# Performance work log

Measured on AMD Instinct MI355X. Metric: run time of the kernel, lower is better.

Reference implementation:

```python
import jax, jax.numpy as jnp
import numpy as np

E = 2          # e_layers
DM = 64        # d_model == emb_dim (hardcoded 64 in out_layer)
H = 8          # n_heads
DH = DM // H
DFF = 256      # d_ff
P = 16         # patch_size
STRIDE = P // 2
SL = 4096      # seq_len
NPATCH = (SL - P) // STRIDE + 1   # 511
PRED = 96
B, M = 8, 8
FACTOR = 5
EPS = 1e-5


def setup_inputs() -> dict:
    key = jax.random.key(0)
    ks = jax.random.split(key, 32)
    s = jnp.float32(0.02)
    f = lambda i, shape: jax.random.normal(ks[i], shape, jnp.float32)
    d = {
        "x_enc": f(0, (B, SL, M)),
        "x_mark_enc": f(1, (B, SL, 4)),
        "x_dec": f(2, (B, PRED, M)),
        "x_mark_dec": f(3, (B, PRED, 4)),
        # patch embedding  Linear(patch_size -> emb_dim)
        "in_W": f(4, (DM, P)) * s,
        "in_b": jnp.zeros((DM,), jnp.float32),
        # per-layer attention projections (stacked over e_layers)
        "Wq": f(5, (E, DM, DM)) * s, "bq": jnp.zeros((E, DM), jnp.float32),
        "Wk": f(6, (E, DM, DM)) * s, "bk": jnp.zeros((E, DM), jnp.float32),
        "Wv": f(7, (E, DM, DM)) * s, "bv": jnp.zeros((E, DM), jnp.float32),
        "Wo": f(8, (E, DM, DM)) * s, "bo": jnp.zeros((E, DM), jnp.float32),
        # FFN (Conv1d kernel=1 == Linear)
        "c1_W": f(9, (E, DFF, DM)) * s, "c1_b": jnp.zeros((E, DFF), jnp.float32),
        "c2_W": f(10, (E, DM, DFF)) * s, "c2_b": jnp.zeros((E, DM), jnp.float32),
        # layer norms
        "ln1_g": jnp.ones((E, DM), jnp.float32), "ln1_b": jnp.zeros((E, DM), jnp.float32),
        "ln2_g": jnp.ones((E, DM), jnp.float32), "ln2_b": jnp.zeros((E, DM), jnp.float32),
        "lnf_g": jnp.ones((DM,), jnp.float32), "lnf_b": jnp.zeros((DM,), jnp.float32),
        # decode head  Linear(64*num_patches -> pred_len)
        "out_W": f(11, (PRED, DM * NPATCH)) * s,
        "out_b": jnp.zeros((PRED,), jnp.float32),
    }
    return d


def _ln(x, g, b):
    mu = x.mean(-1, keepdims=True)
    var = ((x - mu) ** 2).mean(-1, keepdims=True)
    return (x - mu) * jax.lax.rsqrt(var + EPS) * g + b


def _prob_attn(q, k, v, key):
    # q,k,v: [Bn, H, L, Dh]  (ProbSparse attention, mask_flag=False)
    Bn, h, Lq, Dh = q.shape
    Lk = k.shape[2]
    U_part = min(int(FACTOR * np.ceil(np.log(Lk))), Lk)   # sampled keys per query
    u = min(int(FACTOR * np.ceil(np.log(Lq))), Lq)        # top-u active queries
    idx = jax.random.randint(key, (Lq, U_part), 0, Lk)
    k_sample = k[:, :, idx, :]                             # [Bn,H,Lq,U,Dh]
    qk_sample = jnp.einsum('bhld,bhlud->bhlu', q, k_sample)
    # sparsity measure: max - sum/L_K (as in torch code)
    sparsity = qk_sample.max(-1) - qk_sample.sum(-1) / jnp.float32(Lk)
    _, top_idx = jax.lax.top_k(sparsity, u)                # [Bn,H,u]
    q_red = jnp.take_along_axis(q, top_idx[..., None], axis=2)  # [Bn,H,u,Dh]
    scale = jax.lax.rsqrt(jnp.float32(Dh))
    scores = jnp.einsum('bhud,bhkd->bhuk', q_red, k) * scale    # [Bn,H,u,Lk]
    attn = jax.nn.softmax(scores, axis=-1)
    # lazy context: mean of V for inactive queries, attn@V for active ones
    ctx = jnp.broadcast_to(v.mean(axis=2, keepdims=True), q.shape)
    upd = jnp.einsum('bhuk,bhkd->bhud', attn, v)
    bi = jnp.arange(Bn)[:, None, None]
    hi = jnp.arange(h)[None, :, None]
    ctx = ctx.at[bi, hi, top_idx].set(upd)
    return ctx.transpose(0, 2, 1, 3)  # [Bn,L,H,Dh]


def reference(x_enc, x_mark_enc, x_dec, x_mark_dec, in_W, in_b, Wq, bq, Wk, bk,
              Wv, bv, Wo, bo, c1_W, c1_b, c2_W, c2_b, ln1_g, ln1_b, ln2_g, ln2_b,
              lnf_g, lnf_b, out_W, out_b):
    Bb, L, Mm = x_enc.shape
    x = x_enc.transpose(0, 2, 1)  # b l m -> b m l
    pidx = jnp.arange(NPATCH)[:, None] * STRIDE + jnp.arange(P)[None, :]
    patches = x[:, :, pidx]                         # [B,M,N,P] (unfold)
    z = patches.reshape(Bb * Mm, NPATCH, P) @ in_W.T + in_b  # [BM,N,DM]
    akey = jax.random.key(1)
    for e in range(E):
        q = (z @ Wq[e].T + bq[e]).reshape(Bb * Mm, NPATCH, H, DH).transpose(0, 2, 1, 3)
        k = (z @ Wk[e].T + bk[e]).reshape(Bb * Mm, NPATCH, H, DH).transpose(0, 2, 1, 3)
        v = (z @ Wv[e].T + bv[e]).reshape(Bb * Mm, NPATCH, H, DH).transpose(0, 2, 1, 3)
        ctx = _prob_attn(q, k, v, jax.random.fold_in(akey, e))
        new_x = ctx.reshape(Bb * Mm, NPATCH, DM) @ Wo[e].T + bo[e]
        x1 = _ln(z + new_x, ln1_g[e], ln1_b[e])
        y = jax.nn.gelu(x1 @ c1_W[e].T + c1_b[e], approximate=False)
        y = y @ c2_W[e].T + c2_b[e]
        z = _ln(x1 + y, ln2_g[e], ln2_b[e])
    z = _ln(z, lnf_g, lnf_b)
    out = z.reshape(Bb * Mm, -1) @ out_W.T + out_b   # [BM, pred_len]
    out = out.reshape(Bb, Mm, PRED).transpose(0, 2, 1)  # (b m) l -> b l m
    return out[:, -PRED:, :]
```

## Files before the change

kernel.cpp:

```cpp
#include <hip/hip_runtime.h>
#include <hip/hip_bf16.h>
#include <stdint.h>
#include <math.h>

typedef __hip_bfloat16 bf16;
typedef __attribute__((ext_vector_type(8))) short short8;
typedef __attribute__((ext_vector_type(4))) short short4v;
typedef __attribute__((ext_vector_type(4))) float fx4;

#define NP 511
#define UPART 35
#define NTOK 32704
#define NBITS 17885
#define LN_EPS 1e-5f

__host__ __device__ __forceinline__ void tf2x32(uint32_t k0, uint32_t k1,
                                                uint32_t x0, uint32_t x1,
                                                uint32_t* o0, uint32_t* o1) {
  uint32_t ks2 = k0 ^ k1 ^ 0x1BD11BDAu;
  x0 += k0; x1 += k1;
#define TFR(r) { x0 += x1; x1 = (x1 << (r)) | (x1 >> (32 - (r))); x1 ^= x0; }
  TFR(13) TFR(15) TFR(26) TFR(6)   x0 += k1;  x1 += ks2 + 1u;
  TFR(17) TFR(29) TFR(16) TFR(24)  x0 += ks2; x1 += k0 + 2u;
  TFR(13) TFR(15) TFR(26) TFR(6)   x0 += k0;  x1 += k1 + 3u;
  TFR(17) TFR(29) TFR(16) TFR(24)  x0 += k1;  x1 += ks2 + 4u;
  TFR(13) TFR(15) TFR(26) TFR(6)   x0 += ks2; x1 += k0 + 5u;
#undef TFR
  *o0 = x0; *o1 = x1;
}

__device__ __forceinline__ float ldin(const void* p, int i, int f32) {
  if (f32) return ((const float*)p)[i];
  return __bfloat162float(((const bf16*)p)[i]);
}
__device__ __forceinline__ unsigned short f2bf(float v) {
  uint32_t u = __builtin_bit_cast(uint32_t, v);
  u += 0x7fffu + ((u >> 16) & 1u);
  return (unsigned short)(u >> 16);
}
__device__ __forceinline__ float bfb2f(uint32_t h) {
  uint32_t u = h << 16;
  return __builtin_bit_cast(float, u);
}
__device__ __forceinline__ float lo16(uint32_t w) { return bfb2f(w & 0xFFFFu); }
__device__ __forceinline__ float hi16(uint32_t w) { return bfb2f(w >> 16); }
__device__ __forceinline__ uint32_t pack2(float a, float b) {
  return (uint32_t)f2bf(a) | ((uint32_t)f2bf(b) << 16);
}
__device__ __forceinline__ int lanes_below(unsigned long long m) {
  return __builtin_amdgcn_mbcnt_hi((uint32_t)(m >> 32),
         __builtin_amdgcn_mbcnt_lo((uint32_t)m, 0));
}

__global__ void zero_out_kernel(bf16* __restrict__ out, int n) {
  int i = blockIdx.x * 256 + threadIdx.x;
  if (i < n) out[i] = __float2bfloat16(0.f);
}

__global__ void gen_idx_kernel(int* __restrict__ idxT,
    uint32_t ka0, uint32_t ka1, uint32_t kb0, uint32_t kb1,
    const uint32_t* __restrict__ lnfg, int* __restrict__ flag) {
  if (blockIdx.x == 0 && threadIdx.x == 0)
    flag[0] = (lnfg[0] == 0x3F800000u) ? 1 : 0;
  int i = blockIdx.x * 256 + threadIdx.x;
  if (i >= 2 * NBITS) return;
  int e = i / NBITS;
  uint32_t j = (uint32_t)(i - e * NBITS);
  uint32_t k0 = e ? kb0 : ka0, k1 = e ? kb1 : ka1;
  uint32_t o0, o1;
  tf2x32(k0, k1, 0u, j, &o0, &o1);
  uint32_t bits = o1;
  uint32_t hi = bits >> 16, lo = bits & 0xFFFFu;
  uint32_t off = ((hi % 511u) * 32u + (lo % 511u)) % 511u;
  int l = (int)(j / UPART), u = (int)(j % UPART);
  idxT[e * NBITS + u * NP + l] = (int)off;
}

__global__ __launch_bounds__(256) void embed_kernel(
    const void* __restrict__ xe, const void* __restrict__ inW,
    const void* __restrict__ inb, float* __restrict__ z,
    const int* __restrict__ flg) {
  __shared__ float xs[136 * 8];
  int f = flg[0];
  int b = blockIdx.x >> 5, nt = blockIdx.x & 31;
  int n0 = nt * 16;
  for (int i = threadIdx.x; i < 1088; i += 256) {
    int row = i >> 3, m = i & 7;
    int g = n0 * 8 + row;
    xs[i] = (g < 4096) ? ldin(xe, (b * 4096 + g) * 8 + m, f) : 0.f;
  }
  int d = threadIdx.x & 63, mg = threadIdx.x >> 6;
  float wreg[16];
#pragma unroll
  for (int p = 0; p < 16; ++p) wreg[p] = ldin(inW, d * 16 + p, f);
  float bd = ldin(inb, d, f);
  __syncthreads();
  for (int nl = 0; nl < 16; ++nl) {
    int n = n0 + nl;
    if (n >= NP) break;
#pragma unroll
    for (int mm = 0; mm < 2; ++mm) {
      int m = mg * 2 + mm;
      float acc = bd;
#pragma unroll
      for (int p = 0; p < 16; ++p)
        acc = fmaf(xs[(nl * 8 + p) * 8 + m], wreg[p], acc);
      int t = (b * 8 + m) * NP + n;
      z[(size_t)t * 64 + d] = acc;
    }
  }
}

__global__ __launch_bounds__(256) void qkv_kernel(
    const float* __restrict__ z,
    const void* __restrict__ Wq, const void* __restrict__ bq,
    const void* __restrict__ Wk, const void* __restrict__ bk,
    const void* __restrict__ Wv, const void* __restrict__ bv,
    bf16* __restrict__ qb, bf16* __restrict__ kb, bf16* __restrict__ vb,
    const int* __restrict__ flg, int e) {
  __shared__ short xb[64 * 72];
  __shared__ short wL[192 * 72];
  __shared__ float bqs[192];
  int f = flg[0];
  int t0 = blockIdx.x * 64;
  int tid = threadIdx.x;
  {
    const float4* xg = (const float4*)(z + (size_t)t0 * 64);
#pragma unroll
    for (int r = 0; r < 4; ++r) {
      int i4 = r * 256 + tid;
      float4 v = xg[i4];
      int t = (i4 * 4) >> 6, d = (i4 * 4) & 63;
      short4v h;
      h.x = (short)f2bf(v.x); h.y = (short)f2bf(v.y);
      h.z = (short)f2bf(v.z); h.w = (short)f2bf(v.w);
      *(short4v*)&xb[t * 72 + d] = h;
    }
  }
  if (!f) {
    const uint4* Wg0 = (const uint4*)((const bf16*)Wq + e * 4096);
    const uint4* Wg1 = (const uint4*)((const bf16*)Wk + e * 4096);
    const uint4* Wg2 = (const uint4*)((const bf16*)Wv + e * 4096);
#pragma unroll
    for (int r = 0; r < 2; ++r) {
      int i = r * 256 + tid;
      int row = i >> 3, c8 = (i & 7) * 8;
      *(uint4*)&wL[row * 72 + c8] = Wg0[i];
      *(uint4*)&wL[(64 + row) * 72 + c8] = Wg1[i];
      *(uint4*)&wL[(128 + row) * 72 + c8] = Wg2[i];
    }
  } else {
#pragma unroll
    for (int r = 0; r < 16; ++r) {
      int i = r * 256 + tid;
      int row = i >> 6, c = i & 63;
      wL[row * 72 + c] = (short)f2bf(((const float*)Wq)[e * 4096 + i]);
      wL[(64 + row) * 72 + c] = (short)f2bf(((const float*)Wk)[e * 4096 + i]);
      wL[(128 + row) * 72 + c] = (short)f2bf(((const float*)Wv)[e * 4096 + i]);
    }
  }
  if (tid < 192) {
    int t3 = tid >> 6, j = tid & 63;
    bqs[tid] = (t3 == 0) ? ldin(bq, e * 64 + j, f)
             : (t3 == 1) ? ldin(bk, e * 64 + j, f)
                         : ldin(bv, e * 64 + j, f);
  }
  __syncthreads();
  int lane = tid & 63, w = tid >> 6;
  int m0 = w * 16, col = lane & 15, quad = lane >> 4;
  short8 a0 = *(const short8*)&xb[(m0 + col) * 72 + quad * 8];
  short8 a1 = *(const short8*)&xb[(m0 + col) * 72 + 32 + quad * 8];
#pragma unroll
  for (int nt = 0; nt < 12; ++nt) {
    fx4 acc = {0.f, 0.f, 0.f, 0.f};
    short8 b0 = *(const short8*)&wL[(nt * 16 + col) * 72 + quad * 8];
    short8 b1 = *(const short8*)&wL[(nt * 16 + col) * 72 + 32 + quad * 8];
    acc = __builtin_amdgcn_mfma_f32_16x16x32_bf16(a0, b0, acc, 0, 0, 0);
    acc = __builtin_amdgcn_mfma_f32_16x16x32_bf16(a1, b1, acc, 0, 0, 0);
    int c = nt * 16 + col;
    int t3 = c >> 6, hd = c & 63, h = hd >> 3, d2 = hd & 7;
    bf16* base = (t3 == 0) ? qb : (t3 == 1) ? kb : vb;
    float bia = bqs[c];
#pragma unroll
    for (int reg = 0; reg < 4; ++reg) {
      int tok = t0 + m0 + quad * 4 + reg;
      int bm = tok / NP, n = tok - bm * NP;
      base[((size_t)(bm * 8 + h) * NP + n) * 8 + d2] =
          __float2bfloat16(acc[reg] + bia);
    }
  }
}

__global__ __launch_bounds__(1024, 8) void attn_fused_kernel(
    const bf16* __restrict__ qg, const bf16* __restrict__ kg,
    const bf16* __restrict__ vg, const int* __restrict__ idxT,
    bf16* __restrict__ ctx) {
  __shared__ uint32_t kkp[NP * 5 + 5];
  __shared__ uint32_t kvp[NP * 5 + 5];
  __shared__ float spars[512];
  __shared__ float mxB_s[512], smB_s[512];
  __shared__ float redv[256];
  __shared__ int topi[UPART];
  __shared__ float vmean[8];
  __shared__ unsigned char selflag[NP + 1];
  int bh = blockIdx.x;
  int bm = bh >> 3, h = bh & 7;
  size_t hb = (size_t)bh * NP * 8;
  int tid = threadIdx.x;
  int lane = tid & 63, wv = tid >> 6;
  if (tid < 512) {
    if (tid < NP) {
      uint4 b = ((const uint4*)(kg + hb))[tid];
      uint32_t* dk = kkp + tid * 5;
      dk[0] = b.x; dk[1] = b.y; dk[2] = b.z; dk[3] = b.w;
    }
  } else {
    int n = tid - 512;
    if (n < NP) {
      uint4 c = ((const uint4*)(vg + hb))[n];
      uint32_t* dv = kvp + n * 5;
      dv[0] = c.x; dv[1] = c.y; dv[2] = c.z; dv[3] = c.w;
    }
  }
  __syncthreads();
  float mxA = -1e30f, smA = 0.f;
  if (tid < NP) {
    int l = tid;
    uint4 a = ((const uint4*)(qg + hb))[l];
    float ql[8];
    ql[0] = lo16(a.x); ql[1] = hi16(a.x);
    ql[2] = lo16(a.y); ql[3] = hi16(a.y);
    ql[4] = lo16(a.z); ql[5] = hi16(a.z);
    ql[6] = lo16(a.w); ql[7] = hi16(a.w);
#pragma unroll 6
    for (int u = 0; u < 18; ++u) {
      int j = idxT[u * NP + l];
      j = ((unsigned)j > 510u) ? 0 : j;
      const uint32_t* kr = kkp + j * 5;
      uint32_t w0 = kr[0], w1 = kr[1], w2 = kr[2], w3 = kr[3];
      float dt = 0.f;
      dt = fmaf(ql[0], lo16(w0), dt); dt = fmaf(ql[1], hi16(w0), dt);
      dt = fmaf(ql[2], lo16(w1), dt); dt = fmaf(ql[3], hi16(w1), dt);
      dt = fmaf(ql[4], lo16(w2), dt); dt = fmaf(ql[5], hi16(w2), dt);
      dt = fmaf(ql[6], lo16(w3), dt); dt = fmaf(ql[7], hi16(w3), dt);
      mxA = fmaxf(mxA, dt); smA += dt;
    }
  } else if (tid >= 512 && tid < 512 + NP) {
    int l = tid - 512;
    uint4 a = ((const uint4*)(qg + hb))[l];
    float ql[8];
    ql[0] = lo16(a.x); ql[1] = hi16(a.x);
    ql[2] = lo16(a.y); ql[3] = hi16(a.y);
    ql[4] = lo16(a.z); ql[5] = hi16(a.z);
    ql[6] = lo16(a.w); ql[7] = hi16(a.w);
    float mxB = -1e30f, smB = 0.f;
#pragma unroll 6
    for (int u = 18; u < 35; ++u) {
      int j = idxT[u * NP + l];
      j = ((unsigned)j > 510u) ? 0 : j;
      const uint32_t* kr = kkp + j * 5;
      uint32_t w0 = kr[0], w1 = kr[1], w2 = kr[2], w3 = kr[3];
      float dt = 0.f;
      dt = fmaf(ql[0], lo16(w0), dt); dt = fmaf(ql[1], hi16(w0), dt);
      dt = fmaf(ql[2], lo16(w1), dt); dt = fmaf(ql[3], hi16(w1), dt);
      dt = fmaf(ql[4], lo16(w2), dt); dt = fmaf(ql[5], hi16(w2), dt);
      dt = fmaf(ql[6], lo16(w3), dt); dt = fmaf(ql[7], hi16(w3), dt);
      mxB = fmaxf(mxB, dt); smB += dt;
    }
    mxB_s[l] = mxB; smB_s[l] = smB;
  }
  __syncthreads();
  if (tid < NP) {
    spars[tid] = fmaxf(mxA, mxB_s[tid]) - (smA + smB_s[tid]) * (1.0f / 511.0f);
  } else if (tid >= 512 && tid < 768) {
    int tt = tid - 512;
    int d = tt & 7, pt = tt >> 3;
    int c = d >> 1, odd = d & 1;
    float s = 0.f;
    for (int n = pt; n < NP; n += 32) {
      uint32_t w = kvp[n * 5 + c];
      s += odd ? hi16(w) : lo16(w);
    }
    redv[tt] = s;
  }
  __syncthreads();
  if (tid < 64) {
    uint32_t key[8];
#pragma unroll
    for (int jj = 0; jj < 8; ++jj) {
      int ll = lane + jj * 64;
      if (ll < NP) {
        uint32_t u = __builtin_bit_cast(uint32_t, spars[ll]);
        key[jj] = (u & 0x80000000u) ? ~u : (u | 0x80000000u);
      } else key[jj] = 0u;
    }
    uint32_t p = 0u;
    for (int b = 31; b >= 0; --b) {
      uint32_t t = p | (1u << b);
      int cnt = 0;
#pragma unroll
      for (int jj = 0; jj < 8; ++jj)
        cnt += __popcll(__ballot(key[jj] >= t));
      if (cnt >= UPART) p = t;
    }
    int c1 = 0;
#pragma unroll
    for (int jj = 0; jj < 8; ++jj)
      c1 += __popcll(__ballot(key[jj] > p));
    int need = UPART - c1;
    int base = 0, taken = 0;
#pragma unroll
    for (int jj = 0; jj < 8; ++jj) {
      int ll = lane + jj * 64;
      bool gt = key[jj] > p;
      bool eq = key[jj] == p;
      unsigned long long meq = __ballot(eq);
      int beq = lanes_below(meq);
      bool sel = gt || (eq && (taken + beq) < need);
      unsigned long long msel = __ballot(sel);
      int pos = base + lanes_below(msel);
      if (sel) topi[pos] = ll;
      if (ll < NP) selflag[ll] = sel ? 1 : 0;
      base += __popcll(msel);
      taken += __popcll(meq);
    }
  } else if (tid >= 64 && tid < 72) {
    int d = tid - 64;
    float s = 0.f;
#pragma unroll
    for (int pt = 0; pt < 32; ++pt) s += redv[pt * 8 + d];
    vmean[d] = s * (1.0f / 511.0f);
  }
  __syncthreads();
  size_t cb = (size_t)bm * (NP * 64) + h * 8;
  if (tid < NP && !selflag[tid]) {
    uint4 pv;
    pv.x = pack2(vmean[0], vmean[1]);
    pv.y = pack2(vmean[2], vmean[3]);
    pv.z = pack2(vmean[4], vmean[5]);
    pv.w = pack2(vmean[6], vmean[7]);
    *(uint4*)(ctx + cb + (size_t)tid * 64) = pv;
  }
  const float scale = 0.35355339059327373f;
  int l0 = topi[wv];
  int l1 = topi[wv + 16];
  bool has3 = (wv + 32) < UPART;
  int l2 = has3 ? topi[wv + 32] : l0;
  l0 = ((unsigned)l0 > 510u) ? 0 : l0;
  l1 = ((unsigned)l1 > 510u) ? 0 : l1;
  l2 = ((unsigned)l2 > 510u) ? 0 : l2;
  const uint4* q4p = (const uint4*)(qg + hb);
  uint4 qv0 = q4p[l0];
  uint4 qv1 = q4p[l1];
  uint4 qv2 = q4p[l2];

  auto process = [&](uint4 a, int lsel) {
    float qs[8];
    qs[0] = lo16(a.x); qs[1] = hi16(a.x);
    qs[2] = lo16(a.y); qs[3] = hi16(a.y);
    qs[4] = lo16(a.z); qs[5] = hi16(a.z);
    qs[6] = lo16(a.w); qs[7] = hi16(a.w);
    float sreg[8];
    float mx = -1e30f;
#pragma unroll
    for (int s = 0; s < 8; ++s) {
      int j = lane + s * 64;
      int jc = (j > 510) ? 0 : j;
      const uint32_t* kr = kkp + jc * 5;
      uint32_t w0 = kr[0], w1 = kr[1], w2 = kr[2], w3 = kr[3];
      float d0 = qs[0] * lo16(w0);
      d0 = fmaf(qs[1], hi16(w0), d0);
      d0 = fmaf(qs[2], lo16(w1), d0);
      d0 = fmaf(qs[3], hi16(w1), d0);
      float d1 = qs[4] * lo16(w2);
      d1 = fmaf(qs[5], hi16(w2), d1);
      d1 = fmaf(qs[6], lo16(w3), d1);
      d1 = fmaf(qs[7], hi16(w3), d1);
      float sc = (d0 + d1) * scale;
      sreg[s] = (j > 510) ? -1e30f : sc;
      mx = fmaxf(mx, sreg[s]);
    }
    for (int off = 32; off; off >>= 1) mx = fmaxf(mx, __shfl_xor(mx, off));
    float ssum = 0.f, acc[8];
#pragma unroll
    for (int d2 = 0; d2 < 8; ++d2) acc[d2] = 0.f;
#pragma unroll
    for (int s = 0; s < 8; ++s) {
      int j = lane + s * 64;
      int jc = (j > 510) ? 0 : j;
      float w = __expf(sreg[s] - mx);
      ssum += w;
      const uint32_t* vr = kvp + jc * 5;
      uint32_t x0 = vr[0], x1 = vr[1], x2 = vr[2], x3 = vr[3];
      acc[0] = fmaf(w, lo16(x0), acc[0]); acc[1] = fmaf(w, hi16(x0), acc[1]);
      acc[2] = fmaf(w, lo16(x1), acc[2]); acc[3] = fmaf(w, hi16(x1), acc[3]);
      acc[4] = fmaf(w, lo16(x2), acc[4]); acc[5] = fmaf(w, hi16(x2), acc[5]);
      acc[6] = fmaf(w, lo16(x3), acc[6]); acc[7] = fmaf(w, hi16(x3), acc[7]);
    }
    for (int off = 32; off; off >>= 1) {
      ssum += __shfl_xor(ssum, off);
#pragma unroll
      for (int d2 = 0; d2 < 8; ++d2) acc[d2] += __shfl_xor(acc[d2], off);
    }
    if (lane == 0) {
      float inv = 1.0f / ssum;
      uint4 pv;
      pv.x = pack2(acc[0] * inv, acc[1] * inv);
      pv.y = pack2(acc[2] * inv, acc[3] * inv);
      pv.z = pack2(acc[4] * inv, acc[5] * inv);
      pv.w = pack2(acc[6] * inv, acc[7] * inv);
      *(uint4*)(ctx + cb + (size_t)lsel * 64) = pv;
    }
  };
  process(qv0, l0);
  process(qv1, l1);
  if (has3) process(qv2, l2);
}

__global__ __launch_bounds__(256) void oproj_ffn_kernel(
    const float* __restrict__ z, const bf16* __restrict__ ctx,
    const void* __restrict__ Wo, const void* __restrict__ bo,
    const void* __restrict__ l1g, const void* __restrict__ l1b,
    const void* __restrict__ W1, const void* __restrict__ b1,
    const void* __restrict__ W2, const void* __restrict__ b2,
    const void* __restrict__ g, const void* __restrict__ bb,
    float* __restrict__ zo, bf16* __restrict__ zfT,
    const void* __restrict__ lfg, const void* __restrict__ lfb,
    const int* __restrict__ flg, int e, int last) {
  __shared__ __align__(16) char smem[73728];
  short* cbL = (short*)smem;
  short* woL = (short*)(smem + 9216);
  float* zf  = (float*)(smem + 18432);
  short* wA  = (short*)smem;
  short* rB  = (short*)(smem + 36864);
  float* b1s = (float*)(smem + 70656);
  float* b2s  = b1s + 256;
  float* gs   = b2s + 64;
  float* bbs  = gs + 64;
  float* g2s  = bbs + 64;
  float* bb2s = g2s + 64;
  float* bos  = bb2s + 64;
  float* g1s  = bos + 64;
  float* bb1s = g1s + 64;
  int f = flg[0];
  int t0 = blockIdx.x * 64;
  int tid = threadIdx.x;
  {
    const uint4* cg = (const uint4*)(ctx + (size_t)t0 * 64);
#pragma unroll
    for (int r = 0; r < 2; ++r) {
      int i = r * 256 + tid;
      uint4 v = cg[i];
      int row = i >> 3, c8 = (i & 7) * 8;
      *(uint4*)&cbL[row * 72 + c8] = v;
    }
    const float4* zg = (const float4*)(z + (size_t)t0 * 64);
#pragma unroll
    for (int r = 0; r < 4; ++r) {
      int i4 = r * 256 + tid;
      float4 v = zg[i4];
      int t = (i4 * 4) >> 6, d = (i4 * 4) & 63;
      *(float4*)&zf[t * 64 + d] = v;
    }
  }
  if (!f) {
    const uint4* Wg = (const uint4*)((const bf16*)Wo + e * 4096);
#pragma unroll
    for (int r = 0; r < 2; ++r) {
      int i = r * 256 + tid;
      int row = i >> 3, c8 = (i & 7) * 8;
      *(uint4*)&woL[row * 72 + c8] = Wg[i];
    }
  } else {
#pragma unroll
    for (int r = 0; r < 16; ++r) {
      int i = r * 256 + tid;
      int row = i >> 6, c = i & 63;
      woL[row * 72 + c] = (short)f2bf(((const float*)Wo)[e * 4096 + i]);
    }
  }
  b1s[tid] = ldin(b1, e * 256 + tid, f);
  if (tid < 64) {
    b2s[tid] = ldin(b2, e * 64 + tid, f);
    gs[tid] = ldin(g, e * 64 + tid, f);
    bbs[tid] = ldin(bb, e * 64 + tid, f);
    g2s[tid] = ldin(lfg, tid, f);
    bb2s[tid] = ldin(lfb, tid, f);
    bos[tid] = ldin(bo, e * 64 + tid, f);
    g1s[tid] = ldin(l1g, e * 64 + tid, f);
    bb1s[tid] = ldin(l1b, e * 64 + tid, f);
  }
  __syncthreads();
  int lane = tid & 63, w = tid >> 6;
  int m0 = w * 16, col = lane & 15, quad = lane >> 4;
  float x1v[4][4];
  {
    short8 a0 = *(const short8*)&cbL[(m0 + col) * 72 + quad * 8];
    short8 a1 = *(const short8*)&cbL[(m0 + col) * 72 + 32 + quad * 8];
    fx4 vacc[4];
#pragma unroll
    for (int nt = 0; nt < 4; ++nt) {
      fx4 acc = {0.f, 0.f, 0.f, 0.f};
      short8 b0 = *(const short8*)&woL[(nt * 16 + col) * 72 + quad * 8];
      short8 b1f = *(const short8*)&woL[(nt * 16 + col) * 72 + 32 + quad * 8];
      acc = __builtin_amdgcn_mfma_f32_16x16x32_bf16(a0, b0, acc, 0, 0, 0);
      acc = __builtin_amdgcn_mfma_f32_16x16x32_bf16(a1, b1f, acc, 0, 0, 0);
      vacc[nt] = acc;
    }
    float vals[4][4];
    float ps[4], sq[4];
#pragma unroll
    for (int reg = 0; reg < 4; ++reg) { ps[reg] = 0.f; sq[reg] = 0.f; }
#pragma unroll
    for (int nt = 0; nt < 4; ++nt) {
      int d = nt * 16 + col;
#pragma unroll
      for (int reg = 0; reg < 4; ++reg) {
        int tl = m0 + quad * 4 + reg;
        float v = vacc[nt][reg] + bos[d] + zf[tl * 64 + d];
        vals[nt][reg] = v;
        ps[reg] += v; sq[reg] += v * v;
      }
    }
#pragma unroll
    for (int off = 1; off < 16; off <<= 1) {
#pragma unroll
      for (int reg = 0; reg < 4; ++reg) {
        ps[reg] += __shfl_xor(ps[reg], off);
        sq[reg] += __shfl_xor(sq[reg], off);
      }
    }
#pragma unroll
    for (int reg = 0; reg < 4; ++reg) {
      float mu = ps[reg] * (1.0f / 64.0f);
      float var = sq[reg] * (1.0f / 64.0f) - mu * mu;
      float rs = rsqrtf(fmaxf(var, 0.f) + LN_EPS);
#pragma unroll
      for (int nt = 0; nt < 4; ++nt) {
        int d = nt * 16 + col;
        x1v[nt][reg] = (vals[nt][reg] - mu) * rs * g1s[d] + bb1s[d];
      }
    }
#pragma unroll
    for (int nt = 0; nt < 4; ++nt) {
#pragma unroll
      for (int reg = 0; reg < 4; ++reg) {
        int tl = m0 + quad * 4 + reg;
        rB[tl * 72 + nt * 16 + col] = (short)f2bf(x1v[nt][reg]);
      }
    }
  }
  __syncthreads();
  if (!f) {
    const uint4* W1g = (const uint4*)((const bf16*)W1 + e * 16384);
#pragma unroll
    for (int r = 0; r < 8; ++r) {
      int i = r * 256 + tid;
      uint4 v = W1g[i];
      int j = i >> 3, k = (i & 7) * 8;
      *(uint4*)&wA[j * 72 + k] = v;
    }
  } else {
    for (int r = 0; r < 64; ++r) {
      int i = r * 256 + tid;
      int j = i >> 6, k = i & 63;
      wA[j * 72 + k] = (short)f2bf(((const float*)W1)[e * 16384 + i]);
    }
  }
  short8 a0 = *(const short8*)&rB[(m0 + col) * 72 + quad * 8];
  short8 a1 = *(const short8*)&rB[(m0 + col) * 72 + 32 + quad * 8];
  __syncthreads();
#pragma unroll 4
  for (int nt = 0; nt < 16; ++nt) {
    fx4 acc = {0.f, 0.f, 0.f, 0.f};
    short8 bf0 = *(const short8*)&wA[(nt * 16 + col) * 72 + quad * 8];
    short8 bf1 = *(const short8*)&wA[(nt * 16 + col) * 72 + 32 + quad * 8];
    acc = __builtin_amdgcn_mfma_f32_16x16x32_bf16(a0, bf0, acc, 0, 0, 0);
    acc = __builtin_amdgcn_mfma_f32_16x16x32_bf16(a1, bf1, acc, 0, 0, 0);
    int j = nt * 16 + col;
    float bj = b1s[j];
#pragma unroll
    for (int reg = 0; reg < 4; ++reg) {
      float a = acc[reg] + bj;
      float ge = 0.5f * a * (1.0f + erff(a * 0.70710678118654752f));
      rB[(m0 + quad * 4 + reg) * 264 + j] = (short)f2bf(ge);
    }
  }
  __syncthreads();
  if (!f) {
    const uint4* W2g = (const uint4*)((const bf16*)W2 + e * 16384);
#pragma unroll
    for (int r = 0; r < 8; ++r) {
      int i = r * 256 + tid;
      uint4 v2 = W2g[i];
      int dd = i >> 5, c = (i & 31) * 8;
      *(uint4*)&wA[dd * 264 + c] = v2;
    }
  } else {
    for (int r = 0; r < 64; ++r) {
      int i = r * 256 + tid;
      int dd = i >> 8, c = i & 255;
      wA[dd * 264 + c] = (short)f2bf(((const float*)W2)[e * 16384 + i]);
    }
  }
  __syncthreads();
  short8 af[8];
#pragma unroll
  for (int kt = 0; kt < 8; ++kt)
    af[kt] = *(const short8*)&rB[(m0 + col) * 264 + kt * 32 + quad * 8];
  fx4 vacc[4];
#pragma unroll
  for (int nt = 0; nt < 4; ++nt) {
    fx4 acc = {0.f, 0.f, 0.f, 0.f};
#pragma unroll
    for (int kt = 0; kt < 8; ++kt) {
      short8 bfr = *(const short8*)&wA[(nt * 16 + col) * 264 + kt * 32 + quad * 8];
      acc = __builtin_amdgcn_mfma_f32_16x16x32_bf16(af[kt], bfr, acc, 0, 0, 0);
    }
    vacc[nt] = acc;
  }
  float vals[4][4];
  float ps[4], sq[4];
#pragma unroll
  for (int reg = 0; reg < 4; ++reg) { ps[reg] = 0.f; sq[reg] = 0.f; }
#pragma unroll
  for (int nt = 0; nt < 4; ++nt) {
    int d = nt * 16 + col;
#pragma unroll
    for (int reg = 0; reg < 4; ++reg) {
      float v = vacc[nt][reg] + b2s[d] + x1v[nt][reg];
      vals[nt][reg] = v;
      ps[reg] += v; sq[reg] += v * v;
    }
  }
#pragma unroll
  for (int off = 1; off < 16; off <<= 1) {
#pragma unroll
    for (int reg = 0; reg < 4; ++reg) {
      ps[reg] += __shfl_xor(ps[reg], off);
      sq[reg] += __shfl_xor(sq[reg], off);
    }
  }
  if (!last) {
#pragma unroll
    for (int reg = 0; reg < 4; ++reg) {
      float mu = ps[reg] * (1.0f / 64.0f);
      float var = sq[reg] * (1.0f / 64.0f) - mu * mu;
      float rs = rsqrtf(fmaxf(var, 0.f) + LN_EPS);
      int tl = m0 + quad * 4 + reg;
#pragma unroll
      for (int nt = 0; nt < 4; ++nt) {
        int d = nt * 16 + col;
        zo[(size_t)(t0 + tl) * 64 + d] = (vals[nt][reg] - mu) * rs * gs[d] + bbs[d];
      }
    }
  } else {
    float ps2[4], sq2[4];
#pragma unroll
    for (int reg = 0; reg < 4; ++reg) { ps2[reg] = 0.f; sq2[reg] = 0.f; }
    float v2s[4][4];
#pragma unroll
    for (int reg = 0; reg < 4; ++reg) {
      float mu = ps[reg] * (1.0f / 64.0f);
      float var = sq[reg] * (1.0f / 64.0f) - mu * mu;
      float rs = rsqrtf(fmaxf(var, 0.f) + LN_EPS);
#pragma unroll
      for (int nt = 0; nt < 4; ++nt) {
        int d = nt * 16 + col;
        float v2 = (vals[nt][reg] - mu) * rs * gs[d] + bbs[d];
        v2s[nt][reg] = v2;
        ps2[reg] += v2; sq2[reg] += v2 * v2;
      }
    }
#pragma unroll
    for (int off = 1; off < 16; off <<= 1) {
#pragma unroll
      for (int reg = 0; reg < 4; ++reg) {
        ps2[reg] += __shfl_xor(ps2[reg], off);
        sq2[reg] += __shfl_xor(sq2[reg], off);
      }
    }
#pragma unroll
    for (int reg = 0; reg < 4; ++reg) {
      float mu = ps2[reg] * (1.0f / 64.0f);
      float var = sq2[reg] * (1.0f / 64.0f) - mu * mu;
      float rs = rsqrtf(fmaxf(var, 0.f) + LN_EPS);
      int tok = t0 + m0 + quad * 4 + reg;
      int bm = tok / NP, n = tok - bm * NP;
#pragma unroll
      for (int nt = 0; nt < 4; ++nt) {
        int d = nt * 16 + col;
        zfT[(size_t)n * 4096 + bm * 64 + d] =
            __float2bfloat16((v2s[nt][reg] - mu) * rs * g2s[d] + bb2s[d]);
      }
    }
  }
}

__global__ __launch_bounds__(256) void head1_kernel(
    const bf16* __restrict__ zfT, const void* __restrict__ W,
    float* __restrict__ partial, const int* __restrict__ flg) {
  __shared__ short aL[64 * 72];
  __shared__ short bL[96 * 72];
  int f = flg[0];
  int n = blockIdx.x;
  int tid = threadIdx.x;
  {
    const uint4* Ag = (const uint4*)(zfT + (size_t)n * 4096);
#pragma unroll
    for (int r = 0; r < 2; ++r) {
      int i = r * 256 + tid;
      uint4 v = Ag[i];
      int row = i >> 3, c = (i & 7) * 8;
      *(uint4*)&aL[row * 72 + c] = v;
    }
  }
  if (!f) {
    const uint4* Wg = (const uint4*)W;
#pragma unroll
    for (int r = 0; r < 3; ++r) {
      int i = r * 256 + tid;
      int p = i >> 3, c8 = i & 7;
      uint4 v = Wg[(size_t)p * 4088 + n * 8 + c8];
      *(uint4*)&bL[p * 72 + c8 * 8] = v;
    }
  } else {
    for (int r = 0; r < 24; ++r) {
      int i = r * 256 + tid;
      int p = i >> 6, c = i & 63;
      bL[p * 72 + c] = (short)f2bf(((const float*)W)[(size_t)p * 32704 + n * 64 + c]);
    }
  }
  __syncthreads();
  int lane = tid & 63, w = tid >> 6;
  int m0 = w * 16, col = lane & 15, quad = lane >> 4;
  short8 a0 = *(const short8*)&aL[(m0 + col) * 72 + quad * 8];
  short8 a1 = *(const short8*)&aL[(m0 + col) * 72 + 32 + quad * 8];
  float* pb = partial + (size_t)n * 6144;
#pragma unroll
  for (int nt = 0; nt < 6; ++nt) {
    fx4 acc = {0.f, 0.f, 0.f, 0.f};
    short8 b0 = *(const short8*)&bL[(nt * 16 + col) * 72 + quad * 8];
    short8 b1 = *(const short8*)&bL[(nt * 16 + col) * 72 + 32 + quad * 8];
    acc = __builtin_amdgcn_mfma_f32_16x16x32_bf16(a0, b0, acc, 0, 0, 0);
    acc = __builtin_amdgcn_mfma_f32_16x16x32_bf16(a1, b1, acc, 0, 0, 0);
#pragma unroll
    for (int reg = 0; reg < 4; ++reg)
      pb[(m0 + quad * 4 + reg) * 96 + nt * 16 + col] = acc[reg];
  }
}

__global__ __launch_bounds__(256) void head2_kernel(
    const float* __restrict__ partial, const void* __restrict__ bias,
    void* __restrict__ out, const int* __restrict__ flg) {
  __shared__ float red[4][64];
  int f = flg[0];
  int lane = threadIdx.x & 63, w = threadIdx.x >> 6;
  int j = blockIdx.x * 64 + lane;
  float acc = 0.f;
  for (int n = w; n < NP; n += 4)
    acc += partial[(size_t)n * 6144 + j];
  red[w][lane] = acc;
  __syncthreads();
  if (w == 0) {
    float s = red[0][lane] + red[1][lane] + red[2][lane] + red[3][lane];
    int bm = j / 96, p = j - bm * 96;
    float val = s + ldin(bias, p, f);
    int b = bm >> 3, m = bm & 7;
    int o = (b * 96 + p) * 8 + m;
    if (f) ((float*)out)[o] = val;
    else   ((bf16*)out)[o] = __float2bfloat16(val);
  }
}

extern "C" void kernel_launch(void* const* d_in, const int* in_sizes, int n_in,
                              void* d_out, int out_size, void* d_ws, size_t ws_size,
                              hipStream_t stream) {
  const void* xe  = d_in[0];
  const void* inW = d_in[4];
  const void* inb = d_in[5];
  const void* Wq  = d_in[6];
  const void* bq  = d_in[7];
  const void* Wk  = d_in[8];
  const void* bk  = d_in[9];
  const void* Wv  = d_in[10];
  const void* bv  = d_in[11];
  const void* Wo  = d_in[12];
  const void* bo  = d_in[13];
  const void* c1W = d_in[14];
  const void* c1b = d_in[15];
  const void* c2W = d_in[16];
  const void* c2b = d_in[17];
  const void* l1g = d_in[18];
  const void* l1b = d_in[19];
  const void* l2g = d_in[20];
  const void* l2b = d_in[21];
  const void* lfg = d_in[22];
  const void* lfb = d_in[23];
  const void* oW  = d_in[24];
  const void* obv = d_in[25];

  const size_t NF = (size_t)NTOK * 64;
  const size_t REQ = (3 * NF + 2 * NBITS + 32) * sizeof(float);
  if (ws_size < REQ) {
    zero_out_kernel<<<(out_size + 255) / 256, 256, 0, stream>>>((bf16*)d_out, out_size);
    return;
  }

  float* z   = (float*)d_ws;
  bf16* ctxb = (bf16*)(z + NF);
  bf16* qb   = (bf16*)(z + NF + NF / 2);
  bf16* kb   = (bf16*)(z + 2 * NF);
  bf16* vb   = (bf16*)(z + 2 * NF + NF / 2);
  int* idxb  = (int*)(z + 3 * NF);
  int* flg   = idxb + 2 * NBITS;
  bf16* zfT  = ctxb;
  float* partial = z;

  uint32_t ke[2][2];
  for (int e = 0; e < 2; ++e)
    tf2x32(0u, 1u, 0u, (uint32_t)e, &ke[e][0], &ke[e][1]);
  gen_idx_kernel<<<(2 * NBITS + 255) / 256, 256, 0, stream>>>(idxb,
      ke[0][0], ke[0][1], ke[1][0], ke[1][1], (const uint32_t*)lfg, flg);

  embed_kernel<<<256, 256, 0, stream>>>(xe, inW, inb, z, flg);
  for (int e = 0; e < 2; ++e) {
    qkv_kernel<<<NTOK / 64, 256, 0, stream>>>(z, Wq, bq, Wk, bk, Wv, bv,
        qb, kb, vb, flg, e);
    attn_fused_kernel<<<512, 1024, 0, stream>>>(qb, kb, vb, idxb + e * NBITS,
        ctxb);
    oproj_ffn_kernel<<<NTOK / 64, 256, 0, stream>>>(z, ctxb, Wo, bo, l1g, l1b,
        c1W, c1b, c2W, c2b, l2g, l2b, z, zfT, lfg, lfb, flg, e, e == 1);
  }
  head1_kernel<<<NP, 256, 0, stream>>>(zfT, oW, partial, flg);
  head2_kernel<<<96, 256, 0, stream>>>(partial, obv, d_out, flg);
}
```

Measured before the change: 298.6 us.

## Merge index generation into embed kernel and halve FFN shared memory footprint

Fuses the random index generation kernel with the patch embedding kernel into one launch, with each block recomputing the dtype flag itself instead of reading it from a prior kernel. The O-proj+FFN kernel keeps the residual z in registers instead of staging it in shared memory. It also splits the W1 and W2 weight loads into two halves of 128 hidden units so LDS drops from 72KB to about 38KB, and adds launch bounds targeting 4 blocks per CU. This trades extra barriers and weight reloads for higher occupancy and one fewer launch.

```diff
diff --git a/kernel.cpp b/kernel.cpp
--- a/kernel.cpp
+++ b/kernel.cpp
@@ -12,6 +12,7 @@
 #define UPART 35
 #define NTOK 32704
 #define NBITS 17885
+#define GENB 140
 #define LN_EPS 1e-5f
 
 __host__ __device__ __forceinline__ void tf2x32(uint32_t k0, uint32_t k1,
@@ -57,32 +58,33 @@
   if (i < n) out[i] = __float2bfloat16(0.f);
 }
 
-__global__ void gen_idx_kernel(int* __restrict__ idxT,
+__global__ __launch_bounds__(256) void genidx_embed_kernel(
+    int* __restrict__ idxT,
     uint32_t ka0, uint32_t ka1, uint32_t kb0, uint32_t kb1,
-    const uint32_t* __restrict__ lnfg, int* __restrict__ flag) {
-  if (blockIdx.x == 0 && threadIdx.x == 0)
-    flag[0] = (lnfg[0] == 0x3F800000u) ? 1 : 0;
-  int i = blockIdx.x * 256 + threadIdx.x;
-  if (i >= 2 * NBITS) return;
-  int e = i / NBITS;
-  uint32_t j = (uint32_t)(i - e * NBITS);
-  uint32_t k0 = e ? kb0 : ka0, k1 = e ? kb1 : ka1;
-  uint32_t o0, o1;
-  tf2x32(k0, k1, 0u, j, &o0, &o1);
-  uint32_t bits = o1;
-  uint32_t hi = bits >> 16, lo = bits & 0xFFFFu;
-  uint32_t off = ((hi % 511u) * 32u + (lo % 511u)) % 511u;
-  int l = (int)(j / UPART), u = (int)(j % UPART);
-  idxT[e * NBITS + u * NP + l] = (int)off;
-}
-
-__global__ __launch_bounds__(256) void embed_kernel(
+    const uint32_t* __restrict__ lnfg, int* __restrict__ flag,
     const void* __restrict__ xe, const void* __restrict__ inW,
-    const void* __restrict__ inb, float* __restrict__ z,
-    const int* __restrict__ flg) {
+    const void* __restrict__ inb, float* __restrict__ z) {
+  if (blockIdx.x < GENB) {
+    if (blockIdx.x == 0 && threadIdx.x == 0)
+      flag[0] = (lnfg[0] == 0x3F800000u) ? 1 : 0;
+    int i = blockIdx.x * 256 + threadIdx.x;
+    if (i >= 2 * NBITS) return;
+    int e = i / NBITS;
+    uint32_t j = (uint32_t)(i - e * NBITS);
+    uint32_t k0 = e ? kb0 : ka0, k1 = e ? kb1 : ka1;
+    uint32_t o0, o1;
+    tf2x32(k0, k1, 0u, j, &o0, &o1);
+    uint32_t bits = o1;
+    uint32_t hi = bits >> 16, lo = bits & 0xFFFFu;
+    uint32_t off = ((hi % 511u) * 32u + (lo % 511u)) % 511u;
+    int l = (int)(j / UPART), u = (int)(j % UPART);
+    idxT[e * NBITS + u * NP + l] = (int)off;
+    return;
+  }
   __shared__ float xs[136 * 8];
-  int f = flg[0];
-  int b = blockIdx.x >> 5, nt = blockIdx.x & 31;
+  int f = (lnfg[0] == 0x3F800000u) ? 1 : 0;
+  int bid = blockIdx.x - GENB;
+  int b = bid >> 5, nt = bid & 31;
   int n0 = nt * 16;
   for (int i = threadIdx.x; i < 1088; i += 256) {
     int row = i >> 3, m = i & 7;
@@ -417,7 +419,7 @@
   if (has3) process(qv2, l2);
 }
 
-__global__ __launch_bounds__(256) void oproj_ffn_kernel(
+__global__ __launch_bounds__(256, 4) void oproj_ffn_kernel(
     const float* __restrict__ z, const bf16* __restrict__ ctx,
     const void* __restrict__ Wo, const void* __restrict__ bo,
     const void* __restrict__ l1g, const void* __restrict__ l1b,
@@ -427,13 +429,12 @@
     float* __restrict__ zo, bf16* __restrict__ zfT,
     const void* __restrict__ lfg, const void* __restrict__ lfb,
     const int* __restrict__ flg, int e, int last) {
-  __shared__ __align__(16) char smem[73728];
+  __shared__ __align__(16) char smem[38400];
   short* cbL = (short*)smem;
   short* woL = (short*)(smem + 9216);
-  float* zf  = (float*)(smem + 18432);
   short* wA  = (short*)smem;
-  short* rB  = (short*)(smem + 36864);
-  float* b1s = (float*)(smem + 70656);
+  short* rB  = (short*)(smem + 18432);
+  float* b1s = (float*)(smem + 35328);
   float* b2s  = b1s + 256;
   float* gs   = b2s + 64;
   float* bbs  = gs + 64;
@@ -445,6 +446,17 @@
   int f = flg[0];
   int t0 = blockIdx.x * 64;
   int tid = threadIdx.x;
+  int lane = tid & 63, w = tid >> 6;
+  int m0 = w * 16, col = lane & 15, quad = lane >> 4;
+  float zres[4][4];
+  {
+    const float* zp = z + ((size_t)(t0 + m0 + quad * 4)) * 64 + col;
+#pragma unroll
+    for (int nt = 0; nt < 4; ++nt)
+#pragma unroll
+      for (int reg = 0; reg < 4; ++reg)
+        zres[nt][reg] = zp[(size_t)reg * 64 + nt * 16];
+  }
   {
     const uint4* cg = (const uint4*)(ctx + (size_t)t0 * 64);
 #pragma unroll
@@ -453,14 +465,6 @@
       uint4 v = cg[i];
       int row = i >> 3, c8 = (i & 7) * 8;
       *(uint4*)&cbL[row * 72 + c8] = v;
-    }
-    const float4* zg = (const float4*)(z + (size_t)t0 * 64);
-#pragma unroll
-    for (int r = 0; r < 4; ++r) {
-      int i4 = r * 256 + tid;
-      float4 v = zg[i4];
-      int t = (i4 * 4) >> 6, d = (i4 * 4) & 63;
-      *(float4*)&zf[t * 64 + d] = v;
     }
   }
   if (!f) {
@@ -491,8 +495,6 @@
     bb1s[tid] = ldin(l1b, e * 64 + tid, f);
   }
   __syncthreads();
-  int lane = tid & 63, w = tid >> 6;
-  int m0 = w * 16, col = lane & 15, quad = lane >> 4;
   float x1v[4][4];
   {
     short8 a0 = *(const short8*)&cbL[(m0 + col) * 72 + quad * 8];
@@ -516,8 +518,7 @@
       int d = nt * 16 + col;
 #pragma unroll
       for (int reg = 0; reg < 4; ++reg) {
-        int tl = m0 + quad * 4 + reg;
-        float v = vacc[nt][reg] + bos[d] + zf[tl * 64 + d];
+        float v = vacc[nt][reg] + bos[d] + zres[nt][reg];
         vals[nt][reg] = v;
         ps[reg] += v; sq[reg] += v * v;
       }
@@ -551,71 +552,138 @@
     }
   }
   __syncthreads();
+  short8 ax0 = *(const short8*)&rB[(m0 + col) * 72 + quad * 8];
+  short8 ax1 = *(const short8*)&rB[(m0 + col) * 72 + 32 + quad * 8];
   if (!f) {
     const uint4* W1g = (const uint4*)((const bf16*)W1 + e * 16384);
 #pragma unroll
-    for (int r = 0; r < 8; ++r) {
+    for (int r = 0; r < 4; ++r) {
       int i = r * 256 + tid;
       uint4 v = W1g[i];
       int j = i >> 3, k = (i & 7) * 8;
       *(uint4*)&wA[j * 72 + k] = v;
     }
   } else {
-    for (int r = 0; r < 64; ++r) {
+    for (int r = 0; r < 32; ++r) {
       int i = r * 256 + tid;
       int j = i >> 6, k = i & 63;
       wA[j * 72 + k] = (short)f2bf(((const float*)W1)[e * 16384 + i]);
     }
   }
-  short8 a0 = *(const short8*)&rB[(m0 + col) * 72 + quad * 8];
-  short8 a1 = *(const short8*)&rB[(m0 + col) * 72 + 32 + quad * 8];
-  __syncthreads();
+  __syncthreads();
+  short* ysH = rB;
 #pragma unroll 4
-  for (int nt = 0; nt < 16; ++nt) {
+  for (int nt = 0; nt < 8; ++nt) {
     fx4 acc = {0.f, 0.f, 0.f, 0.f};
     short8 bf0 = *(const short8*)&wA[(nt * 16 + col) * 72 + quad * 8];
     short8 bf1 = *(const short8*)&wA[(nt * 16 + col) * 72 + 32 + quad * 8];
-    acc = __builtin_amdgcn_mfma_f32_16x16x32_bf16(a0, bf0, acc, 0, 0, 0);
-    acc = __builtin_amdgcn_mfma_f32_16x16x32_bf16(a1, bf1, acc, 0, 0, 0);
+    acc = __builtin_amdgcn_mfma_f32_16x16x32_bf16(ax0, bf0, acc, 0, 0, 0);
+    acc = __builtin_amdgcn_mfma_f32_16x16x32_bf16(ax1, bf1, acc, 0, 0, 0);
     int j = nt * 16 + col;
     float bj = b1s[j];
 #pragma unroll
     for (int reg = 0; reg < 4; ++reg) {
       float a = acc[reg] + bj;
       float ge = 0.5f * a * (1.0f + erff(a * 0.70710678118654752f));
-      rB[(m0 + quad * 4 + reg) * 264 + j] = (short)f2bf(ge);
-    }
-  }
-  __syncthreads();
+      ysH[(m0 + quad * 4 + reg) * 132 + j] = (short)f2bf(ge);
+    }
+  }
+  __syncthreads();
+  short8 af[8];
+#pragma unroll
+  for (int kt = 0; kt < 4; ++kt)
+    af[kt] = *(const short8*)&ysH[(m0 + col) * 132 + kt * 32 + quad * 8];
+  if (!f) {
+    const uint4* W1g = (const uint4*)((const bf16*)W1 + e * 16384 + 8192);
+#pragma unroll
+    for (int r = 0; r < 4; ++r) {
+      int i = r * 256 + tid;
+      uint4 v = W1g[i];
+      int j = i >> 3, k = (i & 7) * 8;
+      *(uint4*)&wA[j * 72 + k] = v;
+    }
+  } else {
+    for (int r = 0; r < 32; ++r) {
+      int i = r * 256 + tid;
+      int j = i >> 6, k = i & 63;
+      wA[j * 72 + k] = (short)f2bf(((const float*)W1)[e * 16384 + 8192 + i]);
+    }
+  }
+  __syncthreads();
+#pragma unroll 4
+  for (int nt = 0; nt < 8; ++nt) {
+    fx4 acc = {0.f, 0.f, 0.f, 0.f};
+    short8 bf0 = *(const short8*)&wA[(nt * 16 + col) * 72 + quad * 8];
+    short8 bf1 = *(const short8*)&wA[(nt * 16 + col) * 72 + 32 + quad * 8];
+    acc = __builtin_amdgcn_mfma_f32_16x16x32_bf16(ax0, bf0, acc, 0, 0, 0);
+    acc = __builtin_amdgcn_mfma_f32_16x16x32_bf16(ax1, bf1, acc, 0, 0, 0);
+    int jl = nt * 16 + col;
+    float bj = b1s[128 + jl];
+#pragma unroll
+    for (int reg = 0; reg < 4; ++reg) {
+      float a = acc[reg] + bj;
+      float ge = 0.5f * a * (1.0f + erff(a * 0.70710678118654752f));
+      ysH[(m0 + quad * 4 + reg) * 132 + jl] = (short)f2bf(ge);
+    }
+  }
+  __syncthreads();
+#pragma unroll
+  for (int kt = 0; kt < 4; ++kt)
+    af[4 + kt] = *(const short8*)&ysH[(m0 + col) * 132 + kt * 32 + quad * 8];
   if (!f) {
     const uint4* W2g = (const uint4*)((const bf16*)W2 + e * 16384);
 #pragma unroll
-    for (int r = 0; r < 8; ++r) {
-      int i = r * 256 + tid;
-      uint4 v2 = W2g[i];
-      int dd = i >> 5, c = (i & 31) * 8;
-      *(uint4*)&wA[dd * 264 + c] = v2;
+    for (int r = 0; r < 4; ++r) {
+      int i = r * 256 + tid;
+      int dd = i >> 4, c16 = i & 15;
+      uint4 v = W2g[dd * 32 + c16];
+      *(uint4*)&wA[dd * 132 + c16 * 8] = v;
     }
   } else {
-    for (int r = 0; r < 64; ++r) {
-      int i = r * 256 + tid;
-      int dd = i >> 8, c = i & 255;
-      wA[dd * 264 + c] = (short)f2bf(((const float*)W2)[e * 16384 + i]);
-    }
-  }
-  __syncthreads();
-  short8 af[8];
-#pragma unroll
-  for (int kt = 0; kt < 8; ++kt)
-    af[kt] = *(const short8*)&rB[(m0 + col) * 264 + kt * 32 + quad * 8];
+    for (int r = 0; r < 32; ++r) {
+      int i = r * 256 + tid;
+      int dd = i >> 7, cl = i & 127;
+      wA[dd * 132 + cl] = (short)f2bf(((const float*)W2)[e * 16384 + dd * 256 + cl]);
+    }
+  }
+  __syncthreads();
   fx4 vacc[4];
 #pragma unroll
   for (int nt = 0; nt < 4; ++nt) {
     fx4 acc = {0.f, 0.f, 0.f, 0.f};
 #pragma unroll
-    for (int kt = 0; kt < 8; ++kt) {
-      short8 bfr = *(const short8*)&wA[(nt * 16 + col) * 264 + kt * 32 + quad * 8];
+    for (int kt = 0; kt < 4; ++kt) {
+      short8 bfr = *(const short8*)&wA[(nt * 16 + col) * 132 + kt * 32 + quad * 8];
       acc = __builtin_amdgcn_mfma_f32_16x16x32_bf16(af[kt], bfr, acc, 0, 0, 0);
+    }
+    vacc[nt] = acc;
+  }
+  __syncthreads();
+  if (!f) {
+    const uint4* W2g = (const uint4*)((const bf16*)W2 + e * 16384);
+#pragma unroll
+    for (int r = 0; r < 4; ++r) {
+      int i = r * 256 + tid;
+      int dd = i >> 4, c16 = i & 15;
+      uint4 v = W2g[dd * 32 + 16 + c16];
+      *(uint4*)&wA[dd * 132 + c16 * 8] = v;
+    }
+  } else {
+    for (int r = 0; r < 32; ++r) {
+      int i = r * 256 + tid;
+      int dd = i >> 7, cl = i & 127;
+      wA[dd * 132 + cl] =
+          (short)f2bf(((const float*)W2)[e * 16384 + dd * 256 + 128 + cl]);
+    }
+  }
+  __syncthreads();
+#pragma unroll
+  for (int nt = 0; nt < 4; ++nt) {
+    fx4 acc = vacc[nt];
+#pragma unroll
+    for (int kt = 0; kt < 4; ++kt) {
+      short8 bfr = *(const short8*)&wA[(nt * 16 + col) * 132 + kt * 32 + quad * 8];
+      acc = __builtin_amdgcn_mfma_f32_16x16x32_bf16(af[4 + kt], bfr, acc, 0, 0, 0);
     }
     vacc[nt] = acc;
   }
@@ -820,10 +888,11 @@
   uint32_t ke[2][2];
   for (int e = 0; e < 2; ++e)
     tf2x32(0u, 1u, 0u, (uint32_t)e, &ke[e][0], &ke[e][1]);
-  gen_idx_kernel<<<(2 * NBITS + 255) / 256, 256, 0, stream>>>(idxb,
-      ke[0][0], ke[0][1], ke[1][0], ke[1][1], (const uint32_t*)lfg, flg);
-
-  embed_kernel<<<256, 256, 0, stream>>>(xe, inW, inb, z, flg);
+
+  genidx_embed_kernel<<<GENB + 256, 256, 0, stream>>>(idxb,
+      ke[0][0], ke[0][1], ke[1][0], ke[1][1], (const uint32_t*)lfg, flg,
+      xe, inW, inb, z);
+
   for (int e = 0; e < 2; ++e) {
     qkv_kernel<<<NTOK / 64, 256, 0, stream>>>(z, Wq, bq, Wk, bk, Wv, bv,
         qb, kb, vb, flg, e);
```

Result: slower. 309.1 us (+3.5%).
